# Kernel optimization log

Hardware: AMD Instinct MI355X
Metric: run time of the kernel (lower is better)

## Reference

```python
import jax, jax.numpy as jnp
import numpy as np

B, L = 256, 256
TAU = 0.01


def setup_inputs() -> dict:
    key = jax.random.key(0)
    k1, k2, k3, k4 = jax.random.split(key, 4)
    x = jax.random.normal(k1, (B, L, B), dtype=jnp.float32)
    target = jax.random.normal(k2, (B, L, B), dtype=jnp.float32)
    mask = jnp.ones((B, L), dtype=jnp.int32)  # prefix-valid mask per query; all clips valid
    query_labels = jax.random.randint(k3, (B,), 0, B, dtype=jnp.int64)
    label_mat = jax.random.randint(k4, (B, B), 0, 2, dtype=jnp.int32)  # label_dict[i] -> row i
    return {"x": x, "target": target, "mask": mask, "query_labels": query_labels, "label_mat": label_mat}


def reference(x, target, mask, query_labels, label_mat):
    # x, target: [B, L, B] (batch, clips, queries); mask: [B(queries), L]
    xs = jax.nn.softmax(x, axis=1)
    ts = jax.nn.softmax(target, axis=1)
    m = (mask > 0).astype(xs.dtype)  # [i(query), l]
    # mask target clips per query i (equivalent to the original's :m prefix slice
    # because mask is a contiguous prefix of valid clips)
    tsm = ts * m.T[None, :, :]  # [c, l, i]
    # sim[i, b, c] = sum_l xs[b, l, i] * ts[c, l, i] * m[i, l]  (per-query B x B matmul)
    sim = jnp.einsum('bli,cli->ibc', xs, tsm)
    logits = sim / TAU
    # original computes -log(exp(n_ji)/sum_c exp(n_jc)) == -log_softmax over c, picked at class i
    logp = jax.nn.log_softmax(logits, axis=-1)  # [i, j, c]
    per = jnp.diagonal(logp, axis1=0, axis2=2)  # per[j, i] = logp[i, j, i]
    loss = -(label_mat.astype(xs.dtype).T * per).sum() / x.shape[0]
    return loss
```

## Files before the change

### kernel.cpp

```cpp
#include <hip/hip_runtime.h>
#include <hip/hip_bf16.h>

#define NB 256
#define NL 256
#define SCALE 100.0f

typedef __attribute__((ext_vector_type(4))) unsigned int u32x4;
typedef __attribute__((ext_vector_type(4))) int i32x4;
typedef __attribute__((ext_vector_type(8))) __bf16 bfrag8;
typedef __attribute__((ext_vector_type(4))) float f32x4;

static __device__ __forceinline__ unsigned int pack2bf(float a, float b) {
  union { float f; unsigned int u; } ua, ub;
  ua.f = a; ub.f = b;
  unsigned int ra = (ua.u + 0x7FFFu + ((ua.u >> 16) & 1u)) >> 16;
  unsigned int rb = (ub.u + 0x7FFFu + ((ub.u >> 16) & 1u)) & 0xFFFF0000u;
  return ra | rb;
}

__global__ __launch_bounds__(1024, 2) void exp_t(
    const float* __restrict__ x, const float* __restrict__ tgt,
    unsigned int* __restrict__ xsT, unsigned int* __restrict__ tsT,
    const int* __restrict__ mask,
    float* __restrict__ sumx, float* __restrict__ sumt)
{
  const int b = blockIdx.x;
  const bool is_t = (blockIdx.y != 0);
  const int tid = threadIdx.x;
  const int i = tid & 255;
  const int h = tid >> 8;
  const float* src = (is_t ? tgt : x) + (size_t)b * (NL * NB) + i;
  unsigned int* dstb = (is_t ? tsT : xsT);

  __shared__ __align__(16) unsigned char stg[256 * 128];
  __shared__ float s_sum[4][256];

  const int r0 = tid >> 3;
  const int c  = tid & 7;

  float tsum = 0.f;

  for (int lc = 0; lc < 4; ++lc) {
    float v[16];
    #pragma unroll
    for (int k = 0; k < 16; ++k)
      v[k] = __expf(src[(size_t)(lc * 64 + h * 16 + k) * NB]);
    #pragma unroll
    for (int k = 0; k < 16; ++k) tsum += v[k];
    if (is_t) {
      const i32x4* mrow = reinterpret_cast<const i32x4*>(mask + i * NL + lc * 64 + h * 16);
      #pragma unroll
      for (int mq = 0; mq < 4; ++mq) {
        i32x4 m = mrow[mq];
        if (m.x <= 0) v[mq * 4 + 0] = 0.f;
        if (m.y <= 0) v[mq * 4 + 1] = 0.f;
        if (m.z <= 0) v[mq * 4 + 2] = 0.f;
        if (m.w <= 0) v[mq * 4 + 3] = 0.f;
      }
    }
    u32x4 p0, p1;
    p0.x = pack2bf(v[0], v[1]);   p0.y = pack2bf(v[2], v[3]);
    p0.z = pack2bf(v[4], v[5]);   p0.w = pack2bf(v[6], v[7]);
    p1.x = pack2bf(v[8], v[9]);   p1.y = pack2bf(v[10], v[11]);
    p1.z = pack2bf(v[12], v[13]); p1.w = pack2bf(v[14], v[15]);
    *reinterpret_cast<u32x4*>(&stg[i * 128 + (((h * 2 + 0) ^ (i & 7)) << 4)]) = p0;
    *reinterpret_cast<u32x4*>(&stg[i * 128 + (((h * 2 + 1) ^ (i & 7)) << 4)]) = p1;
    __syncthreads();
    u32x4 q0 = *reinterpret_cast<const u32x4*>(&stg[r0 * 128 + ((c ^ (r0 & 7)) << 4)]);
    u32x4 q1 = *reinterpret_cast<const u32x4*>(&stg[(r0 + 128) * 128 + ((c ^ ((r0 + 128) & 7)) << 4)]);
    *reinterpret_cast<u32x4*>(dstb + ((size_t)b * 256 + r0) * 128 + lc * 32 + c * 4) = q0;
    *reinterpret_cast<u32x4*>(dstb + ((size_t)b * 256 + r0 + 128) * 128 + lc * 32 + c * 4) = q1;
    __syncthreads();
  }

  s_sum[h][i] = tsum;
  __syncthreads();
  if (h == 0) {
    float* so = is_t ? sumt : sumx;
    so[(size_t)b * 256 + i] = s_sum[0][i] + s_sum[1][i] + s_sum[2][i] + s_sum[3][i];
  }
}

__global__ __launch_bounds__(256, 2) void gemm_lse(
    const unsigned short* __restrict__ xsT,
    const unsigned short* __restrict__ tsT,
    const float* __restrict__ sumx,
    const float* __restrict__ sumt,
    const int* __restrict__ label_mat,
    float* __restrict__ out)
{
  const int n  = blockIdx.x;
  const int g  = n & 7;
  const int q  = n >> 3;
  const int i  = ((q >> 2) << 3) + g;
  const int jt = q & 3;
  const int t  = threadIdx.x;
  const int w  = t >> 6;
  const int lane = t & 63;

  __shared__ __align__(16) unsigned char As[64 * 128];
  __shared__ __align__(16) unsigned char Bs[256 * 128];
  __shared__ float s_irx[64];
  __shared__ float s_ict[256];
  __shared__ float s_rmax[4][64];
  __shared__ float s_rsum[4][64];
  __shared__ float s_diag[64];

  const int srow = t >> 3;
  const int sch  = t & 7;

  s_ict[t] = __builtin_amdgcn_rcpf(sumt[(size_t)t * 256 + i]);
  if (t < 64)
    s_irx[t] = SCALE * __builtin_amdgcn_rcpf(sumx[(size_t)(jt * 64 + t) * 256 + i]);

  f32x4 acc[4][4];
  #pragma unroll
  for (int a = 0; a < 4; ++a)
    #pragma unroll
    for (int cc = 0; cc < 4; ++cc) acc[a][cc] = f32x4{0.f, 0.f, 0.f, 0.f};

  u32x4 areg[2], breg[8];

  auto load_chunk = [&](int kc) {
    const int kofs = kc * 64;
    #pragma unroll
    for (int r = 0; r < 2; ++r) {
      int row = srow + r * 32;
      areg[r] = *reinterpret_cast<const u32x4*>(
          xsT + ((size_t)(jt * 64 + row) * 256 + i) * 256 + kofs + sch * 8);
    }
    #pragma unroll
    for (int r = 0; r < 8; ++r) {
      int row = srow + r * 32;
      breg[r] = *reinterpret_cast<const u32x4*>(
          tsT + ((size_t)row * 256 + i) * 256 + kofs + sch * 8);
    }
  };
  auto store_chunk = [&]() {
    #pragma unroll
    for (int r = 0; r < 2; ++r) {
      int row = srow + r * 32;
      *reinterpret_cast<u32x4*>(&As[row * 128 + ((sch ^ (row & 7)) << 4)]) = areg[r];
    }
    #pragma unroll
    for (int r = 0; r < 8; ++r) {
      int row = srow + r * 32;
      *reinterpret_cast<u32x4*>(&Bs[row * 128 + ((sch ^ (row & 7)) << 4)]) = breg[r];
    }
  };

  load_chunk(0);
  #pragma unroll
  for (int kc = 0; kc < 4; ++kc) {
    store_chunk();
    __syncthreads();
    if (kc < 3) load_chunk(kc + 1);
    #pragma unroll
    for (int kk = 0; kk < 2; ++kk) {
      const int co = kk * 4 + (lane >> 4);
      bfrag8 af[4], bfr[4];
      #pragma unroll
      for (int jf = 0; jf < 4; ++jf) {
        int row = jf * 16 + (lane & 15);
        af[jf] = *reinterpret_cast<const bfrag8*>(
            &As[row * 128 + ((co ^ (row & 7)) << 4)]);
      }
      #pragma unroll
      for (int cf = 0; cf < 4; ++cf) {
        int row = w * 64 + cf * 16 + (lane & 15);
        bfr[cf] = *reinterpret_cast<const bfrag8*>(
            &Bs[row * 128 + ((co ^ (row & 7)) << 4)]);
      }
      #pragma unroll
      for (int jf = 0; jf < 4; ++jf)
        #pragma unroll
        for (int cf = 0; cf < 4; ++cf)
          acc[jf][cf] = __builtin_amdgcn_mfma_f32_16x16x32_bf16(
              af[jf], bfr[cf], acc[jf][cf], 0, 0, 0);
    }
    __syncthreads();
  }

  const int rg = (lane >> 4) << 2;

  float fr[4][4], fc[4];
  #pragma unroll
  for (int jf = 0; jf < 4; ++jf)
    #pragma unroll
    for (int reg = 0; reg < 4; ++reg)
      fr[jf][reg] = s_irx[jf * 16 + rg + reg];
  #pragma unroll
  for (int cf = 0; cf < 4; ++cf)
    fc[cf] = s_ict[w * 64 + cf * 16 + (lane & 15)];
  #pragma unroll
  for (int jf = 0; jf < 4; ++jf)
    #pragma unroll
    for (int cf = 0; cf < 4; ++cf)
      #pragma unroll
      for (int reg = 0; reg < 4; ++reg)
        acc[jf][cf][reg] *= fr[jf][reg] * fc[cf];

  #pragma unroll
  for (int jf = 0; jf < 4; ++jf) {
    #pragma unroll
    for (int reg = 0; reg < 4; ++reg) {
      float m = fmaxf(fmaxf(acc[jf][0][reg], acc[jf][1][reg]),
                      fmaxf(acc[jf][2][reg], acc[jf][3][reg]));
      #pragma unroll
      for (int off = 1; off < 16; off <<= 1) m = fmaxf(m, __shfl_xor(m, off, 64));
      if ((lane & 15) == 0) s_rmax[w][jf * 16 + rg + reg] = m;
    }
  }
  if (w == (i >> 6) && (lane & 15) == (i & 15)) {
    const int cfd = (i >> 4) & 3;
    #pragma unroll
    for (int jf = 0; jf < 4; ++jf) {
      #pragma unroll
      for (int reg = 0; reg < 4; ++reg) {
        float v = acc[jf][0][reg];
        #pragma unroll
        for (int cf = 1; cf < 4; ++cf)
          v = (cfd == cf) ? acc[jf][cf][reg] : v;
        s_diag[jf * 16 + rg + reg] = v;
      }
    }
  }
  __syncthreads();

  #pragma unroll
  for (int jf = 0; jf < 4; ++jf) {
    #pragma unroll
    for (int reg = 0; reg < 4; ++reg) {
      int row = jf * 16 + rg + reg;
      float gm = fmaxf(fmaxf(s_rmax[0][row], s_rmax[1][row]),
                       fmaxf(s_rmax[2][row], s_rmax[3][row]));
      float sE = 0.f;
      #pragma unroll
      for (int cf = 0; cf < 4; ++cf) sE += __expf(acc[jf][cf][reg] - gm);
      #pragma unroll
      for (int off = 1; off < 16; off <<= 1) sE += __shfl_xor(sE, off, 64);
      if ((lane & 15) == 0) s_rsum[w][row] = sE;
    }
  }
  __syncthreads();

  float contrib = 0.f;
  if (t < 64) {
    const int row = t;
    float gm = fmaxf(fmaxf(s_rmax[0][row], s_rmax[1][row]),
                     fmaxf(s_rmax[2][row], s_rmax[3][row]));
    float tot = s_rsum[0][row] + s_rsum[1][row] + s_rsum[2][row] + s_rsum[3][row];
    float lse = __logf(tot) + gm;
    float lbl = (float)label_mat[i * NB + jt * 64 + row];
    contrib = lbl * (s_diag[row] - lse);
  }
  #pragma unroll
  for (int off = 32; off >= 1; off >>= 1) contrib += __shfl_down(contrib, off, 64);
  if (t == 0) atomicAdd(out, contrib * (-1.0f / 256.0f));
}

extern "C" void kernel_launch(void* const* d_in, const int* in_sizes, int n_in,
                              void* d_out, int out_size, void* d_ws, size_t ws_size,
                              hipStream_t stream) {
  const float* x   = (const float*)d_in[0];
  const float* tgt = (const float*)d_in[1];
  const int* mask  = (const int*)d_in[2];
  const int* label_mat = (const int*)d_in[4];
  float* out = (float*)d_out;

  unsigned int* xsT = (unsigned int*)d_ws;
  unsigned int* tsT = xsT + (size_t)NB * NB * NL / 2;
  float* sumx = (float*)(tsT + (size_t)NB * NB * NL / 2);
  float* sumt = sumx + (size_t)NB * NB;

  hipMemsetAsync(out, 0, sizeof(float), stream);
  exp_t<<<dim3(NB, 2), 1024, 0, stream>>>(x, tgt, xsT, tsT, mask, sumx, sumt);
  gemm_lse<<<dim3(1024), 256, 0, stream>>>((const unsigned short*)xsT,
                                           (const unsigned short*)tsT,
                                           sumx, sumt, label_mat, out);
}
```

Before: 80.69 us.

## Split exp/transpose kernel across L-chunks with vectorized loads and atomic sums

```diff
diff --git a/kernel.cpp b/kernel.cpp
--- a/kernel.cpp
+++ b/kernel.cpp
@@ -18,7 +18,7 @@
   return ra | rb;
 }
 
-__global__ __launch_bounds__(1024, 2) void exp_t(
+__global__ __launch_bounds__(256, 4) void exp_t(
     const float* __restrict__ x, const float* __restrict__ tgt,
     unsigned int* __restrict__ xsT, unsigned int* __restrict__ tsT,
     const int* __restrict__ mask,
@@ -26,59 +26,74 @@
 {
   const int b = blockIdx.x;
   const bool is_t = (blockIdx.y != 0);
+  const int lt = blockIdx.z;
   const int tid = threadIdx.x;
-  const int i = tid & 255;
-  const int h = tid >> 8;
-  const float* src = (is_t ? tgt : x) + (size_t)b * (NL * NB) + i;
+  const int w = tid >> 6, lane = tid & 63;
+  const int lbase = lt * 64;
+
+  const f32x4* src4 = reinterpret_cast<const f32x4*>(
+      (is_t ? tgt : x) + (size_t)b * (NL * NB));
   unsigned int* dstb = (is_t ? tsT : xsT);
 
   __shared__ __align__(16) unsigned char stg[256 * 128];
-  __shared__ float s_sum[4][256];
-
-  const int r0 = tid >> 3;
-  const int c  = tid & 7;
-
-  float tsum = 0.f;
-
-  for (int lc = 0; lc < 4; ++lc) {
-    float v[16];
-    #pragma unroll
-    for (int k = 0; k < 16; ++k)
-      v[k] = __expf(src[(size_t)(lc * 64 + h * 16 + k) * NB]);
-    #pragma unroll
-    for (int k = 0; k < 16; ++k) tsum += v[k];
+  __shared__ float s_ps[4][256];
+
+  const int row0 = lane * 4;
+  float psum[4] = {0.f, 0.f, 0.f, 0.f};
+
+  #pragma unroll
+  for (int r = 0; r < 4; ++r) {
+    const int l0 = lbase + r * 16 + w * 4;
+    const int s  = r * 4 + w;
+    f32x4 rv[4];
+    #pragma unroll
+    for (int k = 0; k < 4; ++k)
+      rv[k] = src4[(size_t)(l0 + k) * 64 + lane];
+    float v[4][4];
+    #pragma unroll
+    for (int ii = 0; ii < 4; ++ii)
+      #pragma unroll
+      for (int k = 0; k < 4; ++k) {
+        v[ii][k] = __expf(rv[k][ii]);
+        psum[ii] += v[ii][k];
+      }
     if (is_t) {
-      const i32x4* mrow = reinterpret_cast<const i32x4*>(mask + i * NL + lc * 64 + h * 16);
-      #pragma unroll
-      for (int mq = 0; mq < 4; ++mq) {
-        i32x4 m = mrow[mq];
-        if (m.x <= 0) v[mq * 4 + 0] = 0.f;
-        if (m.y <= 0) v[mq * 4 + 1] = 0.f;
-        if (m.z <= 0) v[mq * 4 + 2] = 0.f;
-        if (m.w <= 0) v[mq * 4 + 3] = 0.f;
-      }
-    }
-    u32x4 p0, p1;
-    p0.x = pack2bf(v[0], v[1]);   p0.y = pack2bf(v[2], v[3]);
-    p0.z = pack2bf(v[4], v[5]);   p0.w = pack2bf(v[6], v[7]);
-    p1.x = pack2bf(v[8], v[9]);   p1.y = pack2bf(v[10], v[11]);
-    p1.z = pack2bf(v[12], v[13]); p1.w = pack2bf(v[14], v[15]);
-    *reinterpret_cast<u32x4*>(&stg[i * 128 + (((h * 2 + 0) ^ (i & 7)) << 4)]) = p0;
-    *reinterpret_cast<u32x4*>(&stg[i * 128 + (((h * 2 + 1) ^ (i & 7)) << 4)]) = p1;
-    __syncthreads();
-    u32x4 q0 = *reinterpret_cast<const u32x4*>(&stg[r0 * 128 + ((c ^ (r0 & 7)) << 4)]);
-    u32x4 q1 = *reinterpret_cast<const u32x4*>(&stg[(r0 + 128) * 128 + ((c ^ ((r0 + 128) & 7)) << 4)]);
-    *reinterpret_cast<u32x4*>(dstb + ((size_t)b * 256 + r0) * 128 + lc * 32 + c * 4) = q0;
-    *reinterpret_cast<u32x4*>(dstb + ((size_t)b * 256 + r0 + 128) * 128 + lc * 32 + c * 4) = q1;
-    __syncthreads();
-  }
-
-  s_sum[h][i] = tsum;
+      #pragma unroll
+      for (int ii = 0; ii < 4; ++ii) {
+        i32x4 m = *reinterpret_cast<const i32x4*>(
+            mask + (size_t)(row0 + ii) * NL + l0);
+        if (m.x <= 0) v[ii][0] = 0.f;
+        if (m.y <= 0) v[ii][1] = 0.f;
+        if (m.z <= 0) v[ii][2] = 0.f;
+        if (m.w <= 0) v[ii][3] = 0.f;
+      }
+    }
+    const int ch   = (s >> 1) ^ (lane & 7);
+    const int half = s & 1;
+    #pragma unroll
+    for (int ii = 0; ii < 4; ++ii) {
+      uint2 pk;
+      pk.x = pack2bf(v[ii][0], v[ii][1]);
+      pk.y = pack2bf(v[ii][2], v[ii][3]);
+      *reinterpret_cast<uint2*>(
+          &stg[(row0 + ii) * 128 + (ch << 4) + half * 8]) = pk;
+    }
+  }
+  #pragma unroll
+  for (int ii = 0; ii < 4; ++ii) s_ps[w][row0 + ii] = psum[ii];
   __syncthreads();
-  if (h == 0) {
-    float* so = is_t ? sumt : sumx;
-    so[(size_t)b * 256 + i] = s_sum[0][i] + s_sum[1][i] + s_sum[2][i] + s_sum[3][i];
-  }
+
+  const int c = tid & 7;
+  #pragma unroll
+  for (int k = 0; k < 8; ++k) {
+    const int row = (tid >> 3) + 32 * k;
+    const int chr = c ^ ((row >> 2) & 7);
+    u32x4 q = *reinterpret_cast<const u32x4*>(&stg[row * 128 + (chr << 4)]);
+    *reinterpret_cast<u32x4*>(
+        dstb + ((size_t)b * 256 + row) * 128 + lt * 32 + c * 4) = q;
+  }
+  float tot = s_ps[0][tid] + s_ps[1][tid] + s_ps[2][tid] + s_ps[3][tid];
+  atomicAdd((is_t ? sumt : sumx) + (size_t)b * 256 + tid, tot);
 }
 
 __global__ __launch_bounds__(256, 2) void gemm_lse(
@@ -274,7 +289,8 @@
   float* sumt = sumx + (size_t)NB * NB;
 
   hipMemsetAsync(out, 0, sizeof(float), stream);
-  exp_t<<<dim3(NB, 2), 1024, 0, stream>>>(x, tgt, xsT, tsT, mask, sumx, sumt);
+  hipMemsetAsync(sumx, 0, 2 * (size_t)NB * NB * sizeof(float), stream);
+  exp_t<<<dim3(NB, 2, 4), 256, 0, stream>>>(x, tgt, xsT, tsT, mask, sumx, sumt);
   gemm_lse<<<dim3(1024), 256, 0, stream>>>((const unsigned short*)xsT,
                                            (const unsigned short*)tsT,
                                            sumx, sumt, label_mat, out);
```

Measured after the change: 85.21 us. 5.6% more time.
